# Optimization experiments

Measured on AMD Instinct MI355X. Metric: run time of the kernel, lower is better.

## Reference

```python
import jax, jax.numpy as jnp
import numpy as np
from jax.ops import segment_sum, segment_max

N = 100_000          # nodes
E = 1_600_000        # directed edges (avg degree 16)
F_IN = 128           # raw node embedding dim
D = 64               # node_encoding
H = 4                # num_heads
GRAPH_LAYERS = 2
FLOW_ITERS = 10
COST_CONST = 1.0     # quadratic cost: c * f^2
NEG_SLOPE = 0.2      # GAT leaky-relu slope
EPS = 1e-9


def setup_inputs() -> dict:
    key = jax.random.key(0)
    ks = jax.random.split(key, 16)
    s = 0.05
    return {
        "demands": jax.random.normal(ks[0], (N, 1), jnp.float32),
        "node_embeddings": jax.random.normal(ks[1], (N, F_IN), jnp.float32),
        "edge_src": jax.random.randint(ks[2], (E,), 0, N),
        "edge_dst": jax.random.randint(ks[3], (E,), 0, N),
        # node encoder MLP (no hidden layers)
        "W_enc": jax.random.normal(ks[4], (F_IN + 1, D), jnp.float32) * s,
        "b_enc": jnp.zeros((D,), jnp.float32),
        # SparseGAT params (shared across graph_layers, matching AUTO_REUSE scope)
        "W_gat": jax.random.normal(ks[5], (H, D, D), jnp.float32) * s,
        "a_src_w": jax.random.normal(ks[6], (H, D), jnp.float32) * s,
        "a_dst_w": jax.random.normal(ks[7], (H, D), jnp.float32) * s,
        "b_gat": jnp.zeros((D,), jnp.float32),
        # Gate (GRU-style convex gate)
        "W_gx": jax.random.normal(ks[8], (D, D), jnp.float32) * s,
        "W_gh": jax.random.normal(ks[9], (D, D), jnp.float32) * s,
        "b_g": jnp.zeros((D,), jnp.float32),
        # decoder to 1 output feature
        "W_dec": jax.random.normal(ks[10], (D, 1), jnp.float32) * s,
        "b_dec": jnp.zeros((1,), jnp.float32),
    }


def _seg_softmax(e, seg, n):
    # numerically stable softmax over entries sharing the same segment (row)
    m = segment_max(e, seg, num_segments=n)
    ex = jnp.exp(e - m[seg])
    den = segment_sum(ex, seg, num_segments=n)
    return ex / (den[seg] + EPS)


def reference(demands, node_embeddings, edge_src, edge_dst,
              W_enc, b_enc, W_gat, a_src_w, a_dst_w, b_gat,
              W_gx, W_gh, b_g, W_dec, b_dec):
    loops = jnp.arange(N, dtype=edge_src.dtype)
    src_sl = jnp.concatenate([edge_src, loops])  # adj + I for GAT
    dst_sl = jnp.concatenate([edge_dst, loops])

    # node encoder: relu(concat([emb, demands]) @ W + b)
    h = jax.nn.relu(jnp.concatenate([node_embeddings, demands], axis=1) @ W_enc + b_enc)

    for _ in range(GRAPH_LAYERS):
        t = jnp.einsum('nd,hde->nhe', h, W_gat)              # [N,H,D]
        ss = jnp.einsum('nhe,he->nh', t, a_src_w)            # [N,H]
        sd = jnp.einsum('nhe,he->nh', t, a_dst_w)
        e = jax.nn.leaky_relu(ss[src_sl] + sd[dst_sl], NEG_SLOPE)  # [E+N,H]
        alpha = _seg_softmax(e, src_sl, N)                   # row-wise attn
        agg = segment_sum(alpha[:, :, None] * t[dst_sl], src_sl, num_segments=N)  # [N,H,D]
        nxt = jax.nn.relu(agg.mean(axis=1) + b_gat)          # average heads
        # gate: convex combination of new and previous state
        z = jax.nn.sigmoid(nxt @ W_gx + h @ W_gh + b_g)
        h = z * nxt + (1.0 - z) * h

    pred = h @ W_dec + b_dec                                 # [N,1]
    # flow_weight_pred = sparse.softmax(adj * pred_weights): row-broadcast then row softmax
    scores = pred[edge_src, 0]                               # [E]
    fw = _seg_softmax(scores, edge_src, N)                   # edge values of flow_weight_pred

    d0 = demands[:, 0]

    def body(_, fv):
        inflow = segment_sum(fv, edge_dst, num_segments=N)   # column sums (axis=0)
        adj_in = jax.nn.relu(inflow - d0)
        return fw * adj_in[edge_src]                         # row-broadcast multiply

    flow = jax.lax.fori_loop(0, FLOW_ITERS, body, fw)
    flow_cost = jnp.sum(COST_CONST * flow * flow)            # quadratic edge cost
    return flow_cost, flow, fw
```

## Files before the change

### kernel.cpp

```cpp
#include <hip/hip_runtime.h>


static constexpr int BLK      = 256;
static constexpr int SCAN_BLK = 1024;
static constexpr int CHUNK    = 4096;
static constexpr int LB       = 9;
static constexpr int BN       = 512;


__global__ void hist_kernel(const int* __restrict__ src, const int* __restrict__ dst,
                            int* __restrict__ counts, int E, int B, int nb, int M) {
    extern __shared__ int lh[];
    const int nbins = 2 * B;
    for (int i = threadIdx.x; i < 4 * nbins; i += blockDim.x) lh[i] = 0;
    __syncthreads();
    int* my = lh + (threadIdx.x >> 6) * nbins;
    int base = blockIdx.x * CHUNK;
    int end  = base + CHUNK < E ? base + CHUNK : E;
    int i4beg = base >> 2, i4end = end >> 2;
    for (int i = i4beg + threadIdx.x; i < i4end; i += blockDim.x) {
        int4 s4 = ((const int4*)src)[i];
        int4 d4 = ((const int4*)dst)[i];
        atomicAdd(&my[d4.x >> LB], 1); atomicAdd(&my[B + (s4.x >> LB)], 1);
        atomicAdd(&my[d4.y >> LB], 1); atomicAdd(&my[B + (s4.y >> LB)], 1);
        atomicAdd(&my[d4.z >> LB], 1); atomicAdd(&my[B + (s4.z >> LB)], 1);
        atomicAdd(&my[d4.w >> LB], 1); atomicAdd(&my[B + (s4.w >> LB)], 1);
    }
    if (blockIdx.x == (int)gridDim.x - 1 && threadIdx.x == 0) {
        for (int e = i4end << 2; e < end; ++e) {
            atomicAdd(&my[dst[e] >> LB], 1);
            atomicAdd(&my[B + (src[e] >> LB)], 1);
        }
    }
    __syncthreads();
    for (int i = threadIdx.x; i < nbins; i += blockDim.x) {
        int s = lh[i] + lh[nbins + i] + lh[2 * nbins + i] + lh[3 * nbins + i];
        if (i < B) counts[i * nb + blockIdx.x] = s;
        else       counts[M + (i - B) * nb + blockIdx.x] = s;
    }
}

__global__ void scan_block_kernel(int* __restrict__ data, int* __restrict__ blocksum, int M2) {
    __shared__ int lds[SCAN_BLK];
    int t = threadIdx.x;
    int i = blockIdx.x * SCAN_BLK + t;
    int v = (i < M2) ? data[i] : 0;
    lds[t] = v;
    __syncthreads();
    for (int off = 1; off < SCAN_BLK; off <<= 1) {
        int tmp = (t >= off) ? lds[t - off] : 0;
        __syncthreads();
        lds[t] += tmp;
        __syncthreads();
    }
    if (i < M2) data[i] = lds[t] - v;
    if (t == SCAN_BLK - 1) blocksum[blockIdx.x] = lds[t];
}

__global__ void scan_partials_kernel(const int* __restrict__ bsum, int* __restrict__ boff, int n) {
    __shared__ int lds[SCAN_BLK];
    __shared__ int carry_s;
    if (threadIdx.x == 0) carry_s = 0;
    __syncthreads();
    for (int base = 0; base < n; base += SCAN_BLK) {
        int i = base + threadIdx.x;
        int v = (i < n) ? bsum[i] : 0;
        lds[threadIdx.x] = v;
        __syncthreads();
        for (int off = 1; off < SCAN_BLK; off <<= 1) {
            int tmp = (threadIdx.x >= off) ? lds[threadIdx.x - off] : 0;
            __syncthreads();
            lds[threadIdx.x] += tmp;
            __syncthreads();
        }
        int incl = lds[threadIdx.x];
        int c = carry_s;
        if (i < n) boff[i] = c + incl - v;
        __syncthreads();
        if (threadIdx.x == SCAN_BLK - 1) carry_s = c + incl;
        __syncthreads();
    }
}

__global__ void fused_scatter_kernel(const int* __restrict__ src, const int* __restrict__ dst,
                                     const int* __restrict__ counts, const int* __restrict__ boff,
                                     unsigned* __restrict__ packed, unsigned short* __restrict__ psrc,
                                     int E, int B, int nb, int M) {
    extern __shared__ int loff[];
    int b = blockIdx.x;
    for (int i = threadIdx.x; i < B; i += blockDim.x) {
        int id  = i * nb + b;
        int id2 = M + i * nb + b;
        loff[i]     = counts[id]  + boff[id >> 10];
        loff[B + i] = counts[id2] + boff[id2 >> 10] - E;
    }
    __syncthreads();
    int base = b * CHUNK;
    int end  = base + CHUNK < E ? base + CHUNK : E;
    int i4beg = base >> 2, i4end = end >> 2;
    for (int i = i4beg + threadIdx.x; i < i4end; i += blockDim.x) {
        int4 s4 = ((const int4*)src)[i];
        int4 d4 = ((const int4*)dst)[i];
        #pragma unroll
        for (int k = 0; k < 4; ++k) {
            int s = (k == 0) ? s4.x : (k == 1) ? s4.y : (k == 2) ? s4.z : s4.w;
            int d = (k == 0) ? d4.x : (k == 1) ? d4.y : (k == 2) ? d4.z : d4.w;
            int pos = atomicAdd(&loff[d >> LB], 1);
            packed[pos] = (unsigned)s | ((unsigned)(d & (BN - 1)) << 17);
            int pos2 = atomicAdd(&loff[B + (s >> LB)], 1);
            psrc[pos2] = (unsigned short)(s & (BN - 1));
        }
    }
    if (b == (int)gridDim.x - 1 && threadIdx.x == 0) {
        for (int e = i4end << 2; e < end; ++e) {
            int s = src[e], d = dst[e];
            int pos = atomicAdd(&loff[d >> LB], 1);
            packed[pos] = (unsigned)s | ((unsigned)(d & (BN - 1)) << 17);
            int pos2 = atomicAdd(&loff[B + (s >> LB)], 1);
            psrc[pos2] = (unsigned short)(s & (BN - 1));
        }
    }
}

__global__ void bucket_kernel(const unsigned short* __restrict__ psrc,
                              const unsigned* __restrict__ packed,
                              const int* __restrict__ counts, const int* __restrict__ boff,
                              float* __restrict__ invdeg, float* __restrict__ rA,
                              int* __restrict__ csr_src, int* __restrict__ row_ptr,
                              int N, int E, int B, int nb, int M) {
    __shared__ int cnt[8 * BN];
    __shared__ int off[BN];
    int t = threadIdx.x, b = blockIdx.x, w = t >> 6;
    int g = (b << LB) + t;
    for (int i = t; i < 8 * BN; i += blockDim.x) cnt[i] = 0;
    __syncthreads();
    int id = M + b * nb;
    int beg = counts[id] + boff[id >> 10] - E;
    int end;
    if (b + 1 < B) { int id2 = M + (b + 1) * nb; end = counts[id2] + boff[id2 >> 10] - E; }
    else end = E;
    for (int e = beg + t; e < end; e += blockDim.x)
        atomicAdd(&cnt[(w << 9) + psrc[e]], 1);
    __syncthreads();
    if (g < N) {
        int tot = 0;
        #pragma unroll
        for (int r = 0; r < 8; ++r) tot += cnt[(r << 9) + t];
        float v = 1.0f / ((float)tot + 1e-9f);
        invdeg[g] = v;
        rA[g] = v;
    }
    __syncthreads();
    for (int i = t; i < 8 * BN; i += blockDim.x) cnt[i] = 0;
    __syncthreads();
    id = b * nb;
    beg = counts[id] + boff[id >> 10];
    if (b + 1 < B) { int id2 = (b + 1) * nb; end = counts[id2] + boff[id2 >> 10]; }
    else end = E;
    for (int e = beg + t; e < end; e += blockDim.x)
        atomicAdd(&cnt[(w << 9) + (packed[e] >> 17)], 1);
    __syncthreads();
    int tot = 0;
    #pragma unroll
    for (int r = 0; r < 8; ++r) tot += cnt[(r << 9) + t];
    off[t] = tot;
    __syncthreads();
    for (int s = 1; s < BN; s <<= 1) {
        int v = (t >= s) ? off[t - s] : 0;
        __syncthreads();
        off[t] += v;
        __syncthreads();
    }
    int excl = beg + off[t] - tot;
    if (g < N) row_ptr[g] = excl;
    {
        int base2 = excl;
        #pragma unroll
        for (int r = 0; r < 8; ++r) { int c = cnt[(r << 9) + t]; cnt[(r << 9) + t] = base2; base2 += c; }
    }
    __syncthreads();
    for (int e = beg + t; e < end; e += blockDim.x) {
        unsigned v = packed[e];
        int pos = atomicAdd(&cnt[(w << 9) + (v >> 17)], 1);
        csr_src[pos] = (int)(v & 0x1FFFFu);
    }
    if (b == 0 && t == 0) row_ptr[N] = E;
}

template <bool LAST>
__global__ void spmv_q_kernel(const int* __restrict__ row_ptr, const int* __restrict__ csr_src,
                              const float* __restrict__ r_in, const float* __restrict__ d0,
                              const float* __restrict__ invdeg, float* __restrict__ r_out,
                              float2* __restrict__ rz_out, int N) {
    int tid = blockIdx.x * blockDim.x + threadIdx.x;
    int n = tid >> 2;
    if (n >= N) return;
    int q = tid & 3;
    int beg = row_ptr[n], end = row_ptr[n + 1];
    int len = end - beg;
    int lo = beg + ((len * q) >> 2);
    int hi = beg + ((len * (q + 1)) >> 2);
    float a = 0.0f;
    for (int j = lo; j < hi; ++j) a += r_in[csr_src[j]];
    a += __shfl_xor(a, 1, 64);
    a += __shfl_xor(a, 2, 64);
    if (q == 0) {
        float inv = invdeg[n];
        float p = a - d0[n];
        p = p > 0.0f ? p : 0.0f;
        if (LAST) rz_out[n] = make_float2(p * inv, inv);
        else      r_out[n] = p * inv;
    }
}

__global__ void final_kernel(const int* __restrict__ src, const float2* __restrict__ rz,
                             float* __restrict__ flow, float* __restrict__ fw,
                             float* __restrict__ partials, int E) {
    int i = blockIdx.x * blockDim.x + threadIdx.x;
    int E4 = E >> 2;
    float f2 = 0.0f;
    if (i < E4) {
        int4 s4 = ((const int4*)src)[i];
        float2 a = rz[s4.x], b = rz[s4.y], c = rz[s4.z], d = rz[s4.w];
        int e = i << 2;
        flow[e] = a.x; flow[e + 1] = b.x; flow[e + 2] = c.x; flow[e + 3] = d.x;
        fw[e]   = a.y; fw[e + 1]   = b.y; fw[e + 2]   = c.y; fw[e + 3]   = d.y;
        f2 = a.x * a.x + b.x * b.x + c.x * c.x + d.x * d.x;
    }
    if (blockIdx.x == 0 && threadIdx.x == 0) {
        for (int e = E4 << 2; e < E; ++e) {
            float2 a = rz[src[e]];
            flow[e] = a.x; fw[e] = a.y;
            f2 += a.x * a.x;
        }
    }
    #pragma unroll
    for (int off = 32; off > 0; off >>= 1) f2 += __shfl_down(f2, off, 64);
    __shared__ float wsum[BLK / 64];
    int lane = threadIdx.x & 63, w = threadIdx.x >> 6;
    if (lane == 0) wsum[w] = f2;
    __syncthreads();
    if (threadIdx.x == 0) {
        float s = 0.0f;
        #pragma unroll
        for (int k = 0; k < BLK / 64; ++k) s += wsum[k];
        partials[blockIdx.x] = s;
    }
}

__global__ void reduce_cost_kernel(const float* __restrict__ partials, float* __restrict__ cost, int n) {
    float s = 0.0f;
    for (int i = threadIdx.x; i < n; i += blockDim.x) s += partials[i];
    #pragma unroll
    for (int off = 32; off > 0; off >>= 1) s += __shfl_down(s, off, 64);
    __shared__ float wsum[16];
    int lane = threadIdx.x & 63, w = threadIdx.x >> 6;
    if (lane == 0) wsum[w] = s;
    __syncthreads();
    if (threadIdx.x == 0) {
        float t = 0.0f;
        for (int k = 0; k < (int)(blockDim.x / 64); ++k) t += wsum[k];
        cost[0] = t;
    }
}

extern "C" void kernel_launch(void* const* d_in, const int* in_sizes, int n_in,
                              void* d_out, int out_size, void* d_ws, size_t ws_size,
                              hipStream_t stream) {
    const float* demands  = (const float*)d_in[0];
    const int*   edge_src = (const int*)d_in[2];
    const int*   edge_dst = (const int*)d_in[3];
    const int N = in_sizes[0];
    const int E = in_sizes[2];

    float* out  = (float*)d_out;
    float* cost = out;
    float* flow = out + 1;
    float* fw   = out + 1 + E;

    const int B   = (N + BN - 1) >> LB;
    const int nb  = (E + CHUNK - 1) / CHUNK;
    const int M   = B * nb;
    const int M2  = 2 * M;
    const int nbs = (M2 + SCAN_BLK - 1) / SCAN_BLK;
    const int gridF = ((E >> 2) + BLK - 1) / BLK;
    const int gridS = (4 * N + BLK - 1) / BLK;

    auto align16 = [](size_t x) { return (x + 15) & ~size_t(15); };
    char* ws = (char*)d_ws;
    size_t o = 0;
    float*    invdeg   = (float*)(ws + o);    o += align16((size_t)N * 4);
    float*    rA       = (float*)(ws + o);    o += align16((size_t)N * 4);
    float*    rB       = (float*)(ws + o);    o += align16((size_t)N * 4);
    float2*   rz2      = (float2*)(ws + o);   o += align16((size_t)N * 8);
    int*      row_ptr  = (int*)(ws + o);      o += align16((size_t)(N + 1) * 4);
    int*      counts   = (int*)(ws + o);      o += align16((size_t)M2 * 4);
    int*      blocksum = (int*)(ws + o);      o += align16((size_t)nbs * 4);
    int*      blockoff = (int*)(ws + o);      o += align16((size_t)nbs * 4);
    unsigned* packed   = (unsigned*)(ws + o); o += align16((size_t)E * 4);
    unsigned short* psrc = (unsigned short*)(ws + o); o += align16((size_t)E * 2);
    int*      csr_src  = (int*)(ws + o);      o += align16((size_t)E * 4);
    float*    partials = (float*)(ws + o);    o += align16((size_t)gridF * 4);

    hist_kernel<<<nb, BLK, (size_t)(8 * B) * 4, stream>>>(edge_src, edge_dst, counts, E, B, nb, M);
    scan_block_kernel<<<nbs, SCAN_BLK, 0, stream>>>(counts, blocksum, M2);
    scan_partials_kernel<<<1, SCAN_BLK, 0, stream>>>(blocksum, blockoff, nbs);
    fused_scatter_kernel<<<nb, BLK, (size_t)(2 * B) * 4, stream>>>(
        edge_src, edge_dst, counts, blockoff, packed, psrc, E, B, nb, M);
    bucket_kernel<<<B, BN, 0, stream>>>(psrc, packed, counts, blockoff,
                                        invdeg, rA, csr_src, row_ptr, N, E, B, nb, M);

    float* r_cur = rA;
    float* r_nxt = rB;
    for (int it = 0; it < 9; ++it) {
        spmv_q_kernel<false><<<gridS, BLK, 0, stream>>>(row_ptr, csr_src, r_cur, demands,
                                                        invdeg, r_nxt, nullptr, N);
        float* t = r_cur; r_cur = r_nxt; r_nxt = t;
    }
    spmv_q_kernel<true><<<gridS, BLK, 0, stream>>>(row_ptr, csr_src, r_cur, demands,
                                                   invdeg, nullptr, rz2, N);

    final_kernel<<<gridF, BLK, 0, stream>>>(edge_src, rz2, flow, fw, partials, E);
    reduce_cost_kernel<<<1, 1024, 0, stream>>>(partials, cost, gridF);
}
```

Baseline: 171.8 us.

## Drop partial-scan kernel, fold block-offset scan into consumers, pack demand with invdeg

The separate single-block scan of block sums is removed. The fused scatter and bucket kernels now each rescan the small blocksum array in shared memory, which saves one launch and its serial dependency. The histogram and scatter kernels move to larger chunks and 512-thread blocks with 8 private histograms, which halves the number of blocks and partial counts. Demand and inverse degree are packed into a float2 so each SpMV step does one load instead of two. The cost is redundant scan work in every block, and the code assumes the block count of the first scan fits in 256 entries.

Result: no change. 170.4 us (-0.8%).

```diff
diff --git a/kernel.cpp b/kernel.cpp
--- a/kernel.cpp
+++ b/kernel.cpp
@@ -2,17 +2,19 @@
 
 
 static constexpr int BLK      = 256;
+static constexpr int BLK_B    = 512;
 static constexpr int SCAN_BLK = 1024;
-static constexpr int CHUNK    = 4096;
+static constexpr int CHUNK    = 8192;
 static constexpr int LB       = 9;
 static constexpr int BN       = 512;
+static constexpr int MAXNBS   = 256;
 
 
 __global__ void hist_kernel(const int* __restrict__ src, const int* __restrict__ dst,
                             int* __restrict__ counts, int E, int B, int nb, int M) {
     extern __shared__ int lh[];
     const int nbins = 2 * B;
-    for (int i = threadIdx.x; i < 4 * nbins; i += blockDim.x) lh[i] = 0;
+    for (int i = threadIdx.x; i < 8 * nbins; i += blockDim.x) lh[i] = 0;
     __syncthreads();
     int* my = lh + (threadIdx.x >> 6) * nbins;
     int base = blockIdx.x * CHUNK;
@@ -34,7 +36,9 @@
     }
     __syncthreads();
     for (int i = threadIdx.x; i < nbins; i += blockDim.x) {
-        int s = lh[i] + lh[nbins + i] + lh[2 * nbins + i] + lh[3 * nbins + i];
+        int s = 0;
+        #pragma unroll
+        for (int r = 0; r < 8; ++r) s += lh[r * nbins + i];
         if (i < B) counts[i * nb + blockIdx.x] = s;
         else       counts[M + (i - B) * nb + blockIdx.x] = s;
     }
@@ -57,48 +61,41 @@
     if (t == SCAN_BLK - 1) blocksum[blockIdx.x] = lds[t];
 }
 
-__global__ void scan_partials_kernel(const int* __restrict__ bsum, int* __restrict__ boff, int n) {
-    __shared__ int lds[SCAN_BLK];
-    __shared__ int carry_s;
-    if (threadIdx.x == 0) carry_s = 0;
-    __syncthreads();
-    for (int base = 0; base < n; base += SCAN_BLK) {
-        int i = base + threadIdx.x;
-        int v = (i < n) ? bsum[i] : 0;
-        lds[threadIdx.x] = v;
-        __syncthreads();
-        for (int off = 1; off < SCAN_BLK; off <<= 1) {
-            int tmp = (threadIdx.x >= off) ? lds[threadIdx.x - off] : 0;
-            __syncthreads();
-            lds[threadIdx.x] += tmp;
-            __syncthreads();
-        }
-        int incl = lds[threadIdx.x];
-        int c = carry_s;
-        if (i < n) boff[i] = c + incl - v;
-        __syncthreads();
-        if (threadIdx.x == SCAN_BLK - 1) carry_s = c + incl;
-        __syncthreads();
-    }
+__device__ __forceinline__ void local_boff_scan(const int* __restrict__ blocksum,
+                                                int* __restrict__ sboff, int nbs, int t) {
+    int own = 0;
+    if (t < MAXNBS) { own = (t < nbs) ? blocksum[t] : 0; sboff[t] = own; }
+    __syncthreads();
+    for (int off = 1; off < MAXNBS; off <<= 1) {
+        int v = (t < MAXNBS && t >= off) ? sboff[t - off] : 0;
+        __syncthreads();
+        if (t < MAXNBS) sboff[t] += v;
+        __syncthreads();
+    }
+    if (t < MAXNBS) sboff[t] -= own;
+    __syncthreads();
 }
 
 __global__ void fused_scatter_kernel(const int* __restrict__ src, const int* __restrict__ dst,
-                                     const int* __restrict__ counts, const int* __restrict__ boff,
+                                     const int* __restrict__ counts, const int* __restrict__ blocksum,
                                      unsigned* __restrict__ packed, unsigned short* __restrict__ psrc,
-                                     int E, int B, int nb, int M) {
-    extern __shared__ int loff[];
-    int b = blockIdx.x;
-    for (int i = threadIdx.x; i < B; i += blockDim.x) {
+                                     int E, int B, int nb, int M, int nbs) {
+    extern __shared__ int smem[];
+    int* loff  = smem;
+    int* sboff = smem + 2 * B;
+    int t = threadIdx.x, b = blockIdx.x;
+    local_boff_scan(blocksum, sboff, nbs, t);
+    for (int i = t; i < B; i += blockDim.x) {
         int id  = i * nb + b;
         int id2 = M + i * nb + b;
-        loff[i]     = counts[id]  + boff[id >> 10];
-        loff[B + i] = counts[id2] + boff[id2 >> 10] - E;
+        loff[i]     = counts[id]  + sboff[id >> 10];
+        loff[B + i] = counts[id2] + sboff[id2 >> 10] - E;
     }
     __syncthreads();
     int base = b * CHUNK;
     int end  = base + CHUNK < E ? base + CHUNK : E;
     int i4beg = base >> 2, i4end = end >> 2;
-    for (int i = i4beg + threadIdx.x; i < i4end; i += blockDim.x) {
+    for (int i = i4beg + t; i < i4end; i += blockDim.x) {
         int4 s4 = ((const int4*)src)[i];
         int4 d4 = ((const int4*)dst)[i];
         #pragma unroll
@@ -111,7 +108,7 @@
             psrc[pos2] = (unsigned short)(s & (BN - 1));
         }
     }
-    if (b == (int)gridDim.x - 1 && threadIdx.x == 0) {
+    if (b == (int)gridDim.x - 1 && t == 0) {
         for (int e = i4end << 2; e < end; ++e) {
             int s = src[e], d = dst[e];
             int pos = atomicAdd(&loff[d >> LB], 1);
@@ -124,20 +121,23 @@
 
 __global__ void bucket_kernel(const unsigned short* __restrict__ psrc,
                               const unsigned* __restrict__ packed,
-                              const int* __restrict__ counts, const int* __restrict__ boff,
-                              float* __restrict__ invdeg, float* __restrict__ rA,
+                              const int* __restrict__ counts, const int* __restrict__ blocksum,
+                              const float* __restrict__ d0,
+                              float2* __restrict__ dz, float* __restrict__ rA,
                               int* __restrict__ csr_src, int* __restrict__ row_ptr,
-                              int N, int E, int B, int nb, int M) {
+                              int N, int E, int B, int nb, int M, int nbs) {
     __shared__ int cnt[8 * BN];
     __shared__ int off[BN];
+    __shared__ int sboff[MAXNBS];
     int t = threadIdx.x, b = blockIdx.x, w = t >> 6;
     int g = (b << LB) + t;
+    local_boff_scan(blocksum, sboff, nbs, t);
     for (int i = t; i < 8 * BN; i += blockDim.x) cnt[i] = 0;
     __syncthreads();
     int id = M + b * nb;
-    int beg = counts[id] + boff[id >> 10] - E;
+    int beg = counts[id] + sboff[id >> 10] - E;
     int end;
-    if (b + 1 < B) { int id2 = M + (b + 1) * nb; end = counts[id2] + boff[id2 >> 10] - E; }
+    if (b + 1 < B) { int id2 = M + (b + 1) * nb; end = counts[id2] + sboff[id2 >> 10] - E; }
     else end = E;
     for (int e = beg + t; e < end; e += blockDim.x)
         atomicAdd(&cnt[(w << 9) + psrc[e]], 1);
@@ -147,15 +147,15 @@
         #pragma unroll
         for (int r = 0; r < 8; ++r) tot += cnt[(r << 9) + t];
         float v = 1.0f / ((float)tot + 1e-9f);
-        invdeg[g] = v;
+        dz[g] = make_float2(d0[g], v);
         rA[g] = v;
     }
     __syncthreads();
     for (int i = t; i < 8 * BN; i += blockDim.x) cnt[i] = 0;
     __syncthreads();
     id = b * nb;
-    beg = counts[id] + boff[id >> 10];
-    if (b + 1 < B) { int id2 = (b + 1) * nb; end = counts[id2] + boff[id2 >> 10]; }
+    beg = counts[id] + sboff[id >> 10];
+    if (b + 1 < B) { int id2 = (b + 1) * nb; end = counts[id2] + sboff[id2 >> 10]; }
     else end = E;
     for (int e = beg + t; e < end; e += blockDim.x)
         atomicAdd(&cnt[(w << 9) + (packed[e] >> 17)], 1);
@@ -189,9 +189,8 @@
 
 template <bool LAST>
 __global__ void spmv_q_kernel(const int* __restrict__ row_ptr, const int* __restrict__ csr_src,
-                              const float* __restrict__ r_in, const float* __restrict__ d0,
-                              const float* __restrict__ invdeg, float* __restrict__ r_out,
-                              float2* __restrict__ rz_out, int N) {
+                              const float* __restrict__ r_in, const float2* __restrict__ dz,
+                              float* __restrict__ r_out, float2* __restrict__ rz_out, int N) {
     int tid = blockIdx.x * blockDim.x + threadIdx.x;
     int n = tid >> 2;
     if (n >= N) return;
@@ -205,11 +204,11 @@
     a += __shfl_xor(a, 1, 64);
     a += __shfl_xor(a, 2, 64);
     if (q == 0) {
-        float inv = invdeg[n];
-        float p = a - d0[n];
+        float2 dzn = dz[n];
+        float p = a - dzn.x;
         p = p > 0.0f ? p : 0.0f;
-        if (LAST) rz_out[n] = make_float2(p * inv, inv);
-        else      r_out[n] = p * inv;
+        if (LAST) rz_out[n] = make_float2(p * dzn.y, dzn.y);
+        else      r_out[n] = p * dzn.y;
     }
 }
 
@@ -289,36 +288,34 @@
     auto align16 = [](size_t x) { return (x + 15) & ~size_t(15); };
     char* ws = (char*)d_ws;
     size_t o = 0;
-    float*    invdeg   = (float*)(ws + o);    o += align16((size_t)N * 4);
+    float2*   dz       = (float2*)(ws + o);   o += align16((size_t)N * 8);
     float*    rA       = (float*)(ws + o);    o += align16((size_t)N * 4);
     float*    rB       = (float*)(ws + o);    o += align16((size_t)N * 4);
     float2*   rz2      = (float2*)(ws + o);   o += align16((size_t)N * 8);
     int*      row_ptr  = (int*)(ws + o);      o += align16((size_t)(N + 1) * 4);
     int*      counts   = (int*)(ws + o);      o += align16((size_t)M2 * 4);
     int*      blocksum = (int*)(ws + o);      o += align16((size_t)nbs * 4);
-    int*      blockoff = (int*)(ws + o);      o += align16((size_t)nbs * 4);
     unsigned* packed   = (unsigned*)(ws + o); o += align16((size_t)E * 4);
     unsigned short* psrc = (unsigned short*)(ws + o); o += align16((size_t)E * 2);
     int*      csr_src  = (int*)(ws + o);      o += align16((size_t)E * 4);
     float*    partials = (float*)(ws + o);    o += align16((size_t)gridF * 4);
 
-    hist_kernel<<<nb, BLK, (size_t)(8 * B) * 4, stream>>>(edge_src, edge_dst, counts, E, B, nb, M);
-    scan_block_kernel<<<nbs, SCAN_BLK, 0, stream>>>(counts, blocksum, M2);
-    scan_partials_kernel<<<1, SCAN_BLK, 0, stream>>>(blocksum, blockoff, nbs);
-    fused_scatter_kernel<<<nb, BLK, (size_t)(2 * B) * 4, stream>>>(
-        edge_src, edge_dst, counts, blockoff, packed, psrc, E, B, nb, M);
-    bucket_kernel<<<B, BN, 0, stream>>>(psrc, packed, counts, blockoff,
-                                        invdeg, rA, csr_src, row_ptr, N, E, B, nb, M);
+    hist_kernel<<<nb, BLK_B, (size_t)(16 * B) * 4, stream>>>(edge_src, edge_dst, counts, E, B, nb, M);
+    scan_block_kernel<<<(M2 + SCAN_BLK - 1) / SCAN_BLK, SCAN_BLK, 0, stream>>>(counts, blocksum, M2);
+    fused_scatter_kernel<<<nb, BLK_B, (size_t)(2 * B + MAXNBS) * 4, stream>>>(
+        edge_src, edge_dst, counts, blocksum, packed, psrc, E, B, nb, M, nbs);
+    bucket_kernel<<<B, BN, 0, stream>>>(psrc, packed, counts, blocksum, demands,
+                                        dz, rA, csr_src, row_ptr, N, E, B, nb, M, nbs);
 
     float* r_cur = rA;
     float* r_nxt = rB;
     for (int it = 0; it < 9; ++it) {
-        spmv_q_kernel<false><<<gridS, BLK, 0, stream>>>(row_ptr, csr_src, r_cur, demands,
-                                                        invdeg, r_nxt, nullptr, N);
+        spmv_q_kernel<false><<<gridS, BLK, 0, stream>>>(row_ptr, csr_src, r_cur, dz,
+                                                        r_nxt, nullptr, N);
         float* t = r_cur; r_cur = r_nxt; r_nxt = t;
     }
-    spmv_q_kernel<true><<<gridS, BLK, 0, stream>>>(row_ptr, csr_src, r_cur, demands,
-                                                   invdeg, nullptr, rz2, N);
+    spmv_q_kernel<true><<<gridS, BLK, 0, stream>>>(row_ptr, csr_src, r_cur, dz,
+                                                   nullptr, rz2, N);
 
     final_kernel<<<gridF, BLK, 0, stream>>>(edge_src, rz2, flow, fw, partials, E);
     reduce_cost_kernel<<<1, 1024, 0, stream>>>(partials, cost, gridF);
```
